# Kernel tuning notes

Measured on AMD Instinct MI355X. Metric: run time of the kernel, lower is better.

The kernel has to match this reference:

```python
import jax, jax.numpy as jnp
import numpy as np

HEADS = 8   # from init_kwargs
K_SIZE = 64

def setup_inputs() -> dict:
    key = jax.random.key(0)
    k1, k2, k3, k4 = jax.random.split(key, 4)
    B, C, D = 4, 2048, 1024
    return {
        "x": jax.random.normal(k1, (B, C, D), dtype=jnp.float32),
        "Mq": jax.random.normal(k2, (D, HEADS * K_SIZE), dtype=jnp.float32) * 0.02,
        "Mk": jax.random.normal(k3, (D, HEADS * K_SIZE), dtype=jnp.float32) * 0.02,
        "Mv": jax.random.normal(k4, (D, 1024), dtype=jnp.float32) * 0.02,
    }

def reference(x, Mq, Mk, Mv):
    B, C, _ = x.shape
    H, K = HEADS, K_SIZE
    V = Mv.shape[1] // H  # v_size = output_size // heads = 128
    # Faithful to torch: (x @ M).view(B, H, C, -1) is a raw row-major reshape
    # of the [B, C, H*K] projection, which mixes token and head axes exactly
    # as the original module does.
    q = (x @ Mq).reshape(B, H, C, K)
    k = (x @ Mk).reshape(B, H, C, K)
    v = (x @ Mv).reshape(B, H, C, V)
    # scores: [B*H, C, C]; scale by sqrt(k_size); softmax over dim=1 (the
    # first C axis), matching the original's unusual softmax dim.
    scores = jnp.einsum('bhqk,bhck->bhqc', q, k).reshape(B * H, C, C)
    att = jax.nn.softmax(scores / jnp.sqrt(jnp.float32(K)), axis=1)
    # att_weights.view(B, C, heads, -1): raw reshape from [B*H, C, C]
    att4 = att.reshape(B, C, H, C)
    # intended semantics of `att4 @ v`: per-head attn-weighted sum of values
    out = jnp.einsum('bqhc,bhcd->bqhd', att4, v)  # [B, C, H, V]
    return out.reshape(B, C, H * V)
```

## Files before the change

kernel.cpp:

```cpp
#include <hip/hip_runtime.h>
#include <stdint.h>
#include <stddef.h>


typedef short     bf8v  __attribute__((ext_vector_type(8)));
typedef float     f4v   __attribute__((ext_vector_type(4)));
typedef unsigned short u16x4 __attribute__((ext_vector_type(4)));
typedef unsigned short u16x8 __attribute__((ext_vector_type(8)));
typedef unsigned int   u32x4 __attribute__((ext_vector_type(4)));

__device__ __forceinline__ unsigned int pk2(float a, float b) {
    union { float f; uint32_t u; } x, y; x.f = a; y.f = b;
    return __builtin_amdgcn_perm(y.u + 0x8000u, x.u + 0x8000u, 0x07060302u);
}

#define MFMA32(A, B, C) __builtin_amdgcn_mfma_f32_16x16x32_bf16((A), (B), (C), 0, 0, 0)
#define ASYNC16(g, l) __builtin_amdgcn_global_load_lds(                        \
    (const __attribute__((address_space(1))) unsigned int*)(g),                \
    (__attribute__((address_space(3))) unsigned int*)(l), 16, 0, 0)

__global__ __launch_bounds__(256) void k_cvt(const float* __restrict__ in,
                                             unsigned short* __restrict__ out, int n4) {
    int i = blockIdx.x * 256 + threadIdx.x;
    if (i >= n4) return;
    f4v v = *(const f4v*)(in + (size_t)i * 4);
    uint2 o; o.x = pk2(v[0], v[1]); o.y = pk2(v[2], v[3]);
    *(uint2*)(out + (size_t)i * 4) = o;
}

__global__ __launch_bounds__(256) void k_cvtT3(const float* __restrict__ Mq,
                                               const float* __restrict__ Mk,
                                               const float* __restrict__ Mv,
                                               unsigned short* __restrict__ wqt,
                                               unsigned short* __restrict__ wkt,
                                               unsigned short* __restrict__ wvt) {
    __shared__ unsigned short t[64][68];
    const int tid = threadIdx.x;
    const int tr = tid >> 4, tc4 = (tid & 15) * 4;
    const float* in; unsigned short* outT; int Ncols, cb;
    if (blockIdx.z == 0) {
        if (blockIdx.x < 8) { in = Mq; outT = wqt; Ncols = 512; cb = blockIdx.x * 64; }
        else                { in = Mk; outT = wkt; Ncols = 512; cb = (blockIdx.x - 8) * 64; }
    } else                  { in = Mv; outT = wvt; Ncols = 1024; cb = blockIdx.x * 64; }
    const int rb = blockIdx.y * 64;
#pragma unroll
    for (int p = 0; p < 4; ++p) {
        int r = tr + p * 16;
        f4v v = *(const f4v*)(in + (size_t)(rb + r) * Ncols + cb + tc4);
        *(unsigned int*)&t[r][tc4]     = pk2(v[0], v[1]);
        *(unsigned int*)&t[r][tc4 + 2] = pk2(v[2], v[3]);
    }
    __syncthreads();
#pragma unroll
    for (int p = 0; p < 4; ++p) {
        int r = tr + p * 16;
        u16x4 o;
        o[0] = t[tc4 + 0][r]; o[1] = t[tc4 + 1][r];
        o[2] = t[tc4 + 2][r]; o[3] = t[tc4 + 3][r];
        *(u16x4*)(outT + (size_t)(cb + r) * 1024 + rb + tc4) = o;
    }
}

__global__ __launch_bounds__(256) void k_T(const unsigned short* __restrict__ in,
                                           unsigned short* __restrict__ out) {
    __shared__ unsigned short t[64][68];
    const int tid = threadIdx.x;
    const int tr = tid >> 4, tc4 = (tid & 15) * 4;
    const int rb = blockIdx.y * 64, cb = blockIdx.x * 64;
    const unsigned short* ib = in  + (size_t)blockIdx.z * 262144;
    unsigned short*       ob = out + (size_t)blockIdx.z * 262144;
#pragma unroll
    for (int p = 0; p < 4; ++p) {
        int r = tr + p * 16;
        u16x4 v = *(const u16x4*)(ib + (size_t)(rb + r) * 128 + cb + tc4);
        t[r][tc4 + 0] = v[0]; t[r][tc4 + 1] = v[1];
        t[r][tc4 + 2] = v[2]; t[r][tc4 + 3] = v[3];
    }
    __syncthreads();
#pragma unroll
    for (int p = 0; p < 4; ++p) {
        int r = tr + p * 16;
        u16x4 o;
        o[0] = t[tc4 + 0][r]; o[1] = t[tc4 + 1][r];
        o[2] = t[tc4 + 2][r]; o[3] = t[tc4 + 3][r];
        *(u16x4*)(ob + (size_t)(cb + r) * 2048 + rb + tc4) = o;
    }
}

__global__ __launch_bounds__(256, 2) void k_gemm(const unsigned short* __restrict__ X,
                                                 const unsigned short* __restrict__ Wt,
                                                 unsigned short* __restrict__ pq,
                                                 unsigned short* __restrict__ pk,
                                                 unsigned short* __restrict__ pv) {
    __shared__ __align__(16) unsigned short smem[32768];
    const int tid = threadIdx.x;
    const int lane = tid & 63, w = tid >> 6;
    const int lc = lane & 15, quad = lane >> 4;
    const int rowb = blockIdx.x * 128, cb = blockIdx.y;

    unsigned short* outp; int N, colb; float scale;
    if (cb < 4)      { outp = pq; N = 512;  colb = cb * 128;       scale = 0.125f; }
    else if (cb < 8) { outp = pk; N = 512;  colb = (cb - 4) * 128; scale = 1.0f; }
    else             { outp = pv; N = 1024; colb = (cb - 8) * 128; scale = 1.0f; }

    const int lr   = lane >> 3;
    const int swz  = ((lane & 7) ^ lr) * 8;

    f4v acc[2][8];
#pragma unroll
    for (int mt = 0; mt < 2; ++mt)
#pragma unroll
        for (int nt = 0; nt < 8; ++nt) acc[mt][nt] = f4v{0.f, 0.f, 0.f, 0.f};

#pragma unroll
    for (int j = 0; j < 4; ++j) {
        int row = (w * 4 + j) * 8 + lr;
        ASYNC16(X  + (size_t)(rowb + row) * 1024 + swz,     &smem[(w * 4 + j) * 512]);
        ASYNC16(Wt + (size_t)(cb * 128 + row) * 1024 + swz, &smem[16384 + (w * 4 + j) * 512]);
    }
    __syncthreads();

    for (int k = 0; k < 16; ++k) {
        const int buf = k & 1;
        const int xoff = buf * 8192, woff = 16384 + buf * 8192;
        if (k < 15) {
            const int k0n = (k + 1) * 64;
            const int nx = (buf ^ 1) * 8192, nw = 16384 + (buf ^ 1) * 8192;
#pragma unroll
            for (int j = 0; j < 4; ++j) {
                int row = (w * 4 + j) * 8 + lr;
                ASYNC16(X  + (size_t)(rowb + row) * 1024 + k0n + swz,     &smem[nx + (w * 4 + j) * 512]);
                ASYNC16(Wt + (size_t)(cb * 128 + row) * 1024 + k0n + swz, &smem[nw + (w * 4 + j) * 512]);
            }
        }
#pragma unroll
        for (int ks = 0; ks < 2; ++ks) {
            bf8v bx[8];
#pragma unroll
            for (int nt = 0; nt < 8; ++nt) {
                int row = nt * 16 + lc;
                int c8  = (ks * 4 + quad) ^ (lc & 7);
                bx[nt] = *(const bf8v*)(&smem[xoff + row * 64 + c8 * 8]);
            }
#pragma unroll
            for (int mt = 0; mt < 2; ++mt) {
                int row = w * 32 + mt * 16 + lc;
                int c8  = (ks * 4 + quad) ^ (lc & 7);
                bf8v a = *(const bf8v*)(&smem[woff + row * 64 + c8 * 8]);
#pragma unroll
                for (int nt = 0; nt < 8; ++nt) acc[mt][nt] = MFMA32(a, bx[nt], acc[mt][nt]);
            }
        }
        __syncthreads();
    }
#pragma unroll
    for (int mt = 0; mt < 2; ++mt)
#pragma unroll
        for (int nt = 0; nt < 8; ++nt) {
            int crow = rowb + nt * 16 + lc;
            int ccol = colb + w * 32 + mt * 16 + quad * 4;
            uint2 o;
            o.x = pk2(acc[mt][nt][0] * scale, acc[mt][nt][1] * scale);
            o.y = pk2(acc[mt][nt][2] * scale, acc[mt][nt][3] * scale);
            *(uint2*)(outp + (size_t)crow * N + ccol) = o;
        }
}

__global__ __launch_bounds__(256, 2) void k_pass1(const unsigned short* __restrict__ Pq,
                                                  const unsigned short* __restrict__ Pk,
                                                  float* __restrict__ rdenl) {
    __shared__ __align__(16) unsigned short kls[8192];
    __shared__ __align__(16) unsigned short qls[2][8192];
    __shared__ float dsum[4][128];
    const int tid = threadIdx.x;
    const int lane = tid & 63, w = tid >> 6;
    const int lc = lane & 15, quad = lane >> 4;
    const int c2b = blockIdx.x * 128;
    const int bg  = blockIdx.y;
    const unsigned short* qbase = Pq + (size_t)bg * 131072;
    const unsigned short* kbase = Pk + (size_t)bg * 131072 + (size_t)c2b * 64;

    const int lr  = lane >> 3;
    const int swz = ((lane & 7) ^ lr) * 8;

#pragma unroll
    for (int j = 0; j < 4; ++j) {
        int row = (w * 4 + j) * 8 + lr;
        ASYNC16(kbase + (size_t)row * 64 + swz, &kls[(w * 4 + j) * 512]);
        ASYNC16(qbase + (size_t)row * 64 + swz, &qls[0][(w * 4 + j) * 512]);
    }
    __syncthreads();

    float csum[8];
#pragma unroll
    for (int nt = 0; nt < 8; ++nt) csum[nt] = 0.f;

    for (int it = 0; it < 16; ++it) {
        const int buf = it & 1;
        if (it < 15) {
            const unsigned short* qn = qbase + (size_t)(it + 1) * 8192;
#pragma unroll
            for (int j = 0; j < 4; ++j) {
                int row = (w * 4 + j) * 8 + lr;
                ASYNC16(qn + (size_t)row * 64 + swz, &qls[buf ^ 1][(w * 4 + j) * 512]);
            }
        }

        f4v sc[2][8];
#pragma unroll
        for (int mt = 0; mt < 2; ++mt)
#pragma unroll
            for (int nt = 0; nt < 8; ++nt) sc[mt][nt] = f4v{0.f, 0.f, 0.f, 0.f};
#pragma unroll
        for (int ks = 0; ks < 2; ++ks) {
            bf8v bk[8];
#pragma unroll
            for (int nt = 0; nt < 8; ++nt) {
                int row = nt * 16 + lc;
                int c8  = (ks * 4 + quad) ^ (lc & 7);
                bk[nt] = *(const bf8v*)(&kls[row * 64 + c8 * 8]);
            }
#pragma unroll
            for (int mt = 0; mt < 2; ++mt) {
                int row = w * 32 + mt * 16 + lc;
                int c8  = (ks * 4 + quad) ^ (lc & 7);
                bf8v a = *(const bf8v*)(&qls[buf][row * 64 + c8 * 8]);
#pragma unroll
                for (int nt = 0; nt < 8; ++nt) sc[mt][nt] = MFMA32(a, bk[nt], sc[mt][nt]);
            }
        }
#pragma unroll
        for (int mt = 0; mt < 2; ++mt)
#pragma unroll
            for (int nt = 0; nt < 8; ++nt)
#pragma unroll
                for (int r = 0; r < 4; ++r)
                    csum[nt] += __expf(sc[mt][nt][r]);
        __syncthreads();
    }

#pragma unroll
    for (int nt = 0; nt < 8; ++nt) {
        float v = csum[nt];
        v += __shfl_xor(v, 16, 64);
        v += __shfl_xor(v, 32, 64);
        if (quad == 0) dsum[w][nt * 16 + lc] = v;
    }
    __syncthreads();
    if (tid < 128) {
        float tot = dsum[0][tid] + dsum[1][tid] + dsum[2][tid] + dsum[3][tid];
        rdenl[(size_t)bg * 2048 + c2b + tid] = -__logf(tot);
    }
}

__global__ __launch_bounds__(256, 2) void k_pass2(const unsigned short* __restrict__ Pq,
                                                  const unsigned short* __restrict__ Pk,
                                                  const unsigned short* __restrict__ Vt,
                                                  const float* __restrict__ rdenl,
                                                  float* __restrict__ out) {
    __shared__ __align__(16) unsigned short kss[2][4096];
    __shared__ __align__(16) unsigned short vs[2][8192];
    const int tid = threadIdx.x;
    const int lane = tid & 63, w = tid >> 6;
    const int lc = lane & 15, quad = lane >> 4;
    const int jt = blockIdx.x, h = blockIdx.y, bg = blockIdx.z;
    const int b = bg >> 3, g = bg & 7;

    const unsigned short* qbase = Pq + (size_t)bg * 131072;
    const unsigned short* kbase = Pk + (size_t)bg * 131072;
    const unsigned short* vbase = Vt + (size_t)(b * 8 + h) * 262144;
    const float* rdl = rdenl + (size_t)bg * 2048;

    bf8v bq[2][2];
#pragma unroll
    for (int nt = 0; nt < 2; ++nt)
#pragma unroll
        for (int ks = 0; ks < 2; ++ks)
            bq[nt][ks] = *(const bf8v*)(qbase +
                (size_t)((jt * 128 + w * 32 + nt * 16 + lc) * 8 + h) * 64 + ks * 32 + quad * 8);

    const int l3 = lane >> 3, l7 = lane & 7;
#pragma unroll
    for (int j = 0; j < 2; ++j) {
        int seg = w * 2 + j;
        int r   = seg * 8 + l3;
        int c   = (l7 - seg - 2 * (l3 & 3)) & 7;
        ASYNC16(kbase + (size_t)r * 64 + c * 8, &kss[0][seg * 512]);
    }
#pragma unroll
    for (int j = 0; j < 4; ++j) {
        int seg = w * 4 + j;
        int d   = seg * 8 + l3;
        int c   = (l7 - l3) & 7;
        ASYNC16(vbase + (size_t)d * 2048 + c * 8, &vs[0][seg * 512]);
    }
    __syncthreads();

    f4v acc[8][2];
#pragma unroll
    for (int dt = 0; dt < 8; ++dt)
#pragma unroll
        for (int nt = 0; nt < 2; ++nt) acc[dt][nt] = f4v{0.f, 0.f, 0.f, 0.f};

    for (int cc = 0; cc < 32; ++cc) {
        const int buf = cc & 1;
        if (cc < 31) {
            const int c2n = (cc + 1) * 64;
#pragma unroll
            for (int j = 0; j < 2; ++j) {
                int seg = w * 2 + j;
                int r   = seg * 8 + l3;
                int c   = (l7 - seg - 2 * (l3 & 3)) & 7;
                ASYNC16(kbase + (size_t)(c2n + r) * 64 + c * 8, &kss[buf ^ 1][seg * 512]);
            }
#pragma unroll
            for (int j = 0; j < 4; ++j) {
                int seg = w * 4 + j;
                int d   = seg * 8 + l3;
                int c   = (l7 - l3) & 7;
                ASYNC16(vbase + (size_t)d * 2048 + c2n + c * 8, &vs[buf ^ 1][seg * 512]);
            }
        }

        f4v sc[4][2];
#pragma unroll
        for (int mt = 0; mt < 4; ++mt)
#pragma unroll
            for (int nt = 0; nt < 2; ++nt) sc[mt][nt] = f4v{0.f, 0.f, 0.f, 0.f};
#pragma unroll
        for (int ks = 0; ks < 2; ++ks) {
            bf8v a[4];
#pragma unroll
            for (int mt = 0; mt < 4; ++mt) {
                int rlog = ((mt >> 1) << 5) + ((lc >> 2) << 3) + ((mt & 1) << 2) + (lc & 3);
                int slot = (ks * 4 + quad + ((mt >> 1) << 2) + (lc >> 2) + 2 * (lc & 3)) & 7;
                a[mt] = *(const bf8v*)(&kss[buf][rlog * 64 + slot * 8]);
            }
#pragma unroll
            for (int mt = 0; mt < 4; ++mt)
#pragma unroll
                for (int nt = 0; nt < 2; ++nt)
                    sc[mt][nt] = MFMA32(a[mt], bq[nt][ks], sc[mt][nt]);
        }

        u32x4 pb[2][2];
#pragma unroll
        for (int mt = 0; mt < 4; ++mt) {
            f4v lrd = *(const f4v*)(rdl + cc * 64 + ((mt >> 1) << 5) + (quad << 3) + ((mt & 1) << 2));
#pragma unroll
            for (int nt = 0; nt < 2; ++nt) {
                float e0 = __expf(sc[mt][nt][0] + lrd[0]);
                float e1 = __expf(sc[mt][nt][1] + lrd[1]);
                float e2 = __expf(sc[mt][nt][2] + lrd[2]);
                float e3 = __expf(sc[mt][nt][3] + lrd[3]);
                pb[mt >> 1][nt][(mt & 1) * 2 + 0] = pk2(e0, e1);
                pb[mt >> 1][nt][(mt & 1) * 2 + 1] = pk2(e2, e3);
            }
        }

#pragma unroll
        for (int kc = 0; kc < 2; ++kc)
#pragma unroll
            for (int dt = 0; dt < 8; ++dt) {
                int dd = dt * 16 + lc;
                int slot = (kc * 4 + quad + (lc & 7)) & 7;
                bf8v a = *(const bf8v*)(&vs[buf][dd * 64 + slot * 8]);
#pragma unroll
                for (int nt = 0; nt < 2; ++nt)
                    acc[dt][nt] = MFMA32(a, *(const bf8v*)&pb[kc][nt], acc[dt][nt]);
            }
        __syncthreads();
    }

    float* ob = out + (size_t)(b * 2048 + g * 256 + jt * 128) * 1024 + h * 128;
#pragma unroll
    for (int dt = 0; dt < 8; ++dt)
#pragma unroll
        for (int nt = 0; nt < 2; ++nt) {
            int r = w * 32 + nt * 16 + lc;
            int d = dt * 16 + quad * 4;
            *(f4v*)(ob + (size_t)r * 1024 + d) = acc[dt][nt];
        }
}

extern "C" void kernel_launch(void* const* d_in, const int* in_sizes, int n_in,
                              void* d_out, int out_size, void* d_ws, size_t ws_size,
                              hipStream_t stream) {
    const float* x  = (const float*)d_in[0];
    const float* Mq = (const float*)d_in[1];
    const float* Mk = (const float*)d_in[2];
    const float* Mv = (const float*)d_in[3];
    float* out = (float*)d_out;

    char* base = (char*)d_ws;
    unsigned short* xb  = (unsigned short*)base;  base += 16777216;
    unsigned short* wqt = (unsigned short*)base;  base += 1048576;
    unsigned short* wkt = (unsigned short*)base;  base += 1048576;
    unsigned short* wvt = (unsigned short*)base;  base += 2097152;
    unsigned short* pq  = (unsigned short*)base;  base += 8388608;
    unsigned short* pk  = (unsigned short*)base;  base += 8388608;
    unsigned short* pv  = (unsigned short*)base;  base += 16777216;
    unsigned short* vt  = (unsigned short*)base;  base += 16777216;
    float* rdenl = (float*)base;                  base += 262144;

    k_cvt<<<8192, 256, 0, stream>>>(x, xb, 2097152);
    k_cvtT3<<<dim3(16, 16, 2), 256, 0, stream>>>(Mq, Mk, Mv, wqt, wkt, wvt);
    k_gemm<<<dim3(64, 16), 256, 0, stream>>>(xb, wqt , pq, pk, pv);
    k_T<<<dim3(2, 32, 32), 256, 0, stream>>>(pv, vt);
    k_pass1<<<dim3(16, 32), 256, 0, stream>>>(pq, pk, rdenl);
    k_pass2<<<dim3(2, 8, 32), 256, 0, stream>>>(pq, pk, vt, rdenl, out);
}
```

Before: 247.9 us.

## Use register-staged K/V prefetch with XOR swizzle, LDS denominators, exp2 softmax

```diff
diff --git a/kernel.cpp b/kernel.cpp
--- a/kernel.cpp
+++ b/kernel.cpp
@@ -99,7 +99,7 @@
     const int rowb = blockIdx.x * 128, cb = blockIdx.y;
 
     unsigned short* outp; int N, colb; float scale;
-    if (cb < 4)      { outp = pq; N = 512;  colb = cb * 128;       scale = 0.125f; }
+    if (cb < 4)      { outp = pq; N = 512;  colb = cb * 128;       scale = 0.18033688011112042f; }
     else if (cb < 8) { outp = pk; N = 512;  colb = (cb - 4) * 128; scale = 1.0f; }
     else             { outp = pv; N = 1024; colb = (cb - 8) * 128; scale = 1.0f; }
 
@@ -235,7 +235,7 @@
             for (int nt = 0; nt < 8; ++nt)
 #pragma unroll
                 for (int r = 0; r < 4; ++r)
-                    csum[nt] += __expf(sc[mt][nt][r]);
+                    csum[nt] += exp2f(sc[mt][nt][r]);
         __syncthreads();
     }
 
@@ -249,7 +249,7 @@
     __syncthreads();
     if (tid < 128) {
         float tot = dsum[0][tid] + dsum[1][tid] + dsum[2][tid] + dsum[3][tid];
-        rdenl[(size_t)bg * 2048 + c2b + tid] = -__logf(tot);
+        rdenl[(size_t)bg * 2048 + c2b + tid] = -log2f(tot);
     }
 }
 
@@ -260,6 +260,7 @@
                                                   float* __restrict__ out) {
     __shared__ __align__(16) unsigned short kss[2][4096];
     __shared__ __align__(16) unsigned short vs[2][8192];
+    __shared__ __align__(16) float rdls[2048];
     const int tid = threadIdx.x;
     const int lane = tid & 63, w = tid >> 6;
     const int lc = lane & 15, quad = lane >> 4;
@@ -279,20 +280,26 @@
             bq[nt][ks] = *(const bf8v*)(qbase +
                 (size_t)((jt * 128 + w * 32 + nt * 16 + lc) * 8 + h) * 64 + ks * 32 + quad * 8);
 
-    const int l3 = lane >> 3, l7 = lane & 7;
-#pragma unroll
-    for (int j = 0; j < 2; ++j) {
-        int seg = w * 2 + j;
-        int r   = seg * 8 + l3;
-        int c   = (l7 - seg - 2 * (l3 & 3)) & 7;
-        ASYNC16(kbase + (size_t)r * 64 + c * 8, &kss[0][seg * 512]);
-    }
-#pragma unroll
-    for (int j = 0; j < 4; ++j) {
-        int seg = w * 4 + j;
-        int d   = seg * 8 + l3;
-        int c   = (l7 - l3) & 7;
-        ASYNC16(vbase + (size_t)d * 2048 + c * 8, &vs[0][seg * 512]);
+    {
+        f4v r0 = *(const f4v*)(rdl + tid * 8);
+        f4v r1 = *(const f4v*)(rdl + tid * 8 + 4);
+        *(f4v*)(&rdls[tid * 8])     = r0;
+        *(f4v*)(&rdls[tid * 8 + 4]) = r1;
+    }
+
+#pragma unroll
+    for (int p = 0; p < 2; ++p) {
+        int v = tid + p * 256;
+        int r = v >> 3, c = v & 7;
+        int slot = c ^ ((r & 3) | (((r >> 3) & 1) << 2));
+        *(u16x8*)(&kss[0][r * 64 + slot * 8]) = *(const u16x8*)(kbase + (size_t)v * 8);
+    }
+#pragma unroll
+    for (int p = 0; p < 4; ++p) {
+        int v = tid + p * 256;
+        int d = v >> 3, c = v & 7;
+        int slot = c ^ (d & 7);
+        *(u16x8*)(&vs[0][d * 64 + slot * 8]) = *(const u16x8*)(vbase + (size_t)d * 2048 + c * 8);
     }
     __syncthreads();
 
@@ -304,21 +311,18 @@
 
     for (int cc = 0; cc < 32; ++cc) {
         const int buf = cc & 1;
+        u16x8 kreg[2], vreg[4];
         if (cc < 31) {
             const int c2n = (cc + 1) * 64;
 #pragma unroll
-            for (int j = 0; j < 2; ++j) {
-                int seg = w * 2 + j;
-                int r   = seg * 8 + l3;
-                int c   = (l7 - seg - 2 * (l3 & 3)) & 7;
-                ASYNC16(kbase + (size_t)(c2n + r) * 64 + c * 8, &kss[buf ^ 1][seg * 512]);
-            }
-#pragma unroll
-            for (int j = 0; j < 4; ++j) {
-                int seg = w * 4 + j;
-                int d   = seg * 8 + l3;
-                int c   = (l7 - l3) & 7;
-                ASYNC16(vbase + (size_t)d * 2048 + c2n + c * 8, &vs[buf ^ 1][seg * 512]);
+            for (int p = 0; p < 2; ++p) {
+                int v = tid + p * 256;
+                kreg[p] = *(const u16x8*)(kbase + (size_t)c2n * 64 + (size_t)v * 8);
+            }
+#pragma unroll
+            for (int p = 0; p < 4; ++p) {
+                int v = tid + p * 256;
+                vreg[p] = *(const u16x8*)(vbase + (size_t)(v >> 3) * 2048 + c2n + (v & 7) * 8);
             }
         }
 
@@ -333,7 +337,8 @@
 #pragma unroll
             for (int mt = 0; mt < 4; ++mt) {
                 int rlog = ((mt >> 1) << 5) + ((lc >> 2) << 3) + ((mt & 1) << 2) + (lc & 3);
-                int slot = (ks * 4 + quad + ((mt >> 1) << 2) + (lc >> 2) + 2 * (lc & 3)) & 7;
+                int fk   = (lc & 3) | (((lc >> 2) & 1) << 2);
+                int slot = (ks * 4 + quad) ^ fk;
                 a[mt] = *(const bf8v*)(&kss[buf][rlog * 64 + slot * 8]);
             }
 #pragma unroll
@@ -346,13 +351,13 @@
         u32x4 pb[2][2];
 #pragma unroll
         for (int mt = 0; mt < 4; ++mt) {
-            f4v lrd = *(const f4v*)(rdl + cc * 64 + ((mt >> 1) << 5) + (quad << 3) + ((mt & 1) << 2));
+            f4v lrd = *(const f4v*)(&rdls[cc * 64 + ((mt >> 1) << 5) + (quad << 3) + ((mt & 1) << 2)]);
 #pragma unroll
             for (int nt = 0; nt < 2; ++nt) {
-                float e0 = __expf(sc[mt][nt][0] + lrd[0]);
-                float e1 = __expf(sc[mt][nt][1] + lrd[1]);
-                float e2 = __expf(sc[mt][nt][2] + lrd[2]);
-                float e3 = __expf(sc[mt][nt][3] + lrd[3]);
+                float e0 = exp2f(sc[mt][nt][0] + lrd[0]);
+                float e1 = exp2f(sc[mt][nt][1] + lrd[1]);
+                float e2 = exp2f(sc[mt][nt][2] + lrd[2]);
+                float e3 = exp2f(sc[mt][nt][3] + lrd[3]);
                 pb[mt >> 1][nt][(mt & 1) * 2 + 0] = pk2(e0, e1);
                 pb[mt >> 1][nt][(mt & 1) * 2 + 1] = pk2(e2, e3);
             }
@@ -363,12 +368,30 @@
 #pragma unroll
             for (int dt = 0; dt < 8; ++dt) {
                 int dd = dt * 16 + lc;
-                int slot = (kc * 4 + quad + (lc & 7)) & 7;
+                int slot = (kc * 4 + quad) ^ (lc & 7);
                 bf8v a = *(const bf8v*)(&vs[buf][dd * 64 + slot * 8]);
 #pragma unroll
                 for (int nt = 0; nt < 2; ++nt)
                     acc[dt][nt] = MFMA32(a, *(const bf8v*)&pb[kc][nt], acc[dt][nt]);
             }
+
+        if (cc < 31) {
+            const int nbuf = buf ^ 1;
+#pragma unroll
+            for (int p = 0; p < 2; ++p) {
+                int v = tid + p * 256;
+                int r = v >> 3, c = v & 7;
+                int slot = c ^ ((r & 3) | (((r >> 3) & 1) << 2));
+                *(u16x8*)(&kss[nbuf][r * 64 + slot * 8]) = kreg[p];
+            }
+#pragma unroll
+            for (int p = 0; p < 4; ++p) {
+                int v = tid + p * 256;
+                int d = v >> 3, c = v & 7;
+                int slot = c ^ (d & 7);
+                *(u16x8*)(&vs[nbuf][d * 64 + slot * 8]) = vreg[p];
+            }
+        }
         __syncthreads();
     }
 
```

Result: slower. 255.0 us (+2.9%).
